# Performance work log

Hardware: AMD Instinct MI355X
Metric: run time of the kernel (lower is better)

## Reference

```python
import jax, jax.numpy as jnp
import numpy as np

K = 7
PAD = K // 2
SIG_L = (4.0, 6.0, 8.0)
SIG_S = (1.0, 2.0, 3.0)
DORD = (0, 1, 2)
ANG = (1, 2, 3, 4)
N_INV, N_EQ, N_CP = 8, 16, 16
LN_EPS = 1e-5


def _polar_grid(k):
    c = jnp.arange(k, dtype=jnp.float32) - (k - 1) / 2.0
    gy, gx = jnp.meshgrid(c, c, indexing='ij')
    r = jnp.sqrt(gx * gx + gy * gy + 1e-8)
    th = jnp.arctan2(gy, gx)
    return r, th


def _gaussian_basis(r, sigmas, orders, n):
    # Gaussian-derivative radial basis (Eqs. 13-14): cycle over (order, sigma) combos.
    combos = [(s, d) for d in orders for s in sigmas]
    mats = []
    for i in range(n):
        s, d = combos[i % len(combos)]
        u = r / s
        g = jnp.exp(-0.5 * u * u)
        p = jnp.ones_like(u) if d == 0 else (u if d == 1 else u * u - 1.0)
        psi = p * g
        mats.append(psi / jnp.sqrt(jnp.sum(psi * psi) + 1e-8))
    return jnp.stack(mats)  # [n, K, K]


def _harmonic_basis(r, th, w1, b1, w2, b2, n):
    # Circular harmonics (Eqs. 15-16): learnable radial MLP x cos/sin(n*theta).
    kk = r.size
    rad = jnp.tanh(r.reshape(kk, 1) @ w1 + b1) @ w2 + b2  # [K*K, M]
    tf = th.reshape(kk)
    ang = jnp.stack([f(o * tf) for o in ANG for f in (jnp.cos, jnp.sin)])  # [2L, K*K]
    basis = (rad.T[:, None, :] * ang[None, :, :]).reshape(-1, K, K)  # [M*2L, K, K]
    return basis[:n]


def _coeff(z, w1, b1, w2, b2, n, cout):
    h = jax.nn.relu(z @ w1 + b1)
    return (h @ w2 + b2).reshape(z.shape[0], n, cout)  # [B, N, C_out]


def _pconv(feature, kernel):
    # Per-sample kernel shared across input channels: conv2d with weight
    # expand over C_in == conv of the channel-sum with the per-(b,o) kernel.
    B, Cin, H, W = feature.shape
    Cout = kernel.shape[1]
    fs = feature.sum(axis=1)[None]  # [1, B, H, W]
    rhs = kernel.reshape(B * Cout, 1, K, K)
    out = jax.lax.conv_general_dilated(fs, rhs, (1, 1), [(PAD, PAD), (PAD, PAD)], feature_group_count=B)
    return out.reshape(B, Cout, H, W)


def _ln_c(x, g, b):
    # LayerNorm over channel dim (permute(0,2,3,1) -> LN -> permute back)
    mu = jnp.mean(x, axis=1, keepdims=True)
    var = jnp.var(x, axis=1, keepdims=True)
    return (x - mu) * jax.lax.rsqrt(var + LN_EPS) * g[None, :, None, None] + b[None, :, None, None]


def setup_inputs() -> dict:
    key = jax.random.key(0)
    ks = jax.random.split(key, 16)
    B, C, H, W = 16, 256, 48, 48
    hid = 64
    d = {}
    d['feature'] = jax.random.normal(ks[0], (B, C, H, W), jnp.float32)
    for i, (name, n) in enumerate([('inv', N_INV), ('eq', N_EQ), ('cp', N_CP)]):
        d[f'cg_{name}_w1'] = jax.random.normal(ks[1 + 4 * i], (C, hid), jnp.float32) * 0.05
        d[f'cg_{name}_b1'] = jnp.zeros((hid,), jnp.float32)
        d[f'cg_{name}_w2'] = jax.random.normal(ks[2 + 4 * i], (hid, n * C), jnp.float32) * 0.05
        d[f'cg_{name}_b2'] = jnp.zeros((n * C,), jnp.float32)
    d['rad_w1'] = jax.random.normal(ks[13], (1, 32), jnp.float32)
    d['rad_b1'] = jnp.zeros((32,), jnp.float32)
    d['rad_w2'] = jax.random.normal(ks[14], (32, 2), jnp.float32) * 0.3
    d['rad_b2'] = jnp.zeros((2,), jnp.float32)
    for name in ('inv', 'eq', 'cp'):
        d[f'ln_{name}_g'] = jnp.ones((C,), jnp.float32)
        d[f'ln_{name}_b'] = jnp.zeros((C,), jnp.float32)
    return d


def reference(feature, cg_inv_w1, cg_inv_b1, cg_inv_w2, cg_inv_b2,
              cg_eq_w1, cg_eq_b1, cg_eq_w2, cg_eq_b2,
              cg_cp_w1, cg_cp_b1, cg_cp_w2, cg_cp_b2,
              rad_w1, rad_b1, rad_w2, rad_b2,
              ln_inv_g, ln_inv_b, ln_eq_g, ln_eq_b, ln_cp_g, ln_cp_b):
    C_out = ln_inv_g.shape[0]
    r, th = _polar_grid(K)
    b_inv = _gaussian_basis(r, SIG_L, DORD, N_INV)
    b_eq = _gaussian_basis(r, SIG_S, DORD, N_EQ)
    b_cp = _harmonic_basis(r, th, rad_w1, rad_b1, rad_w2, rad_b2, N_CP)
    z = feature.mean(axis=(2, 3))  # [B, C] global average pool
    # Eq. 12: kernel[b,c] = sum_n coeff[b,n,c] * basis[n]
    k_inv = jnp.einsum('bnc,nhw->bchw', _coeff(z, cg_inv_w1, cg_inv_b1, cg_inv_w2, cg_inv_b2, N_INV, C_out), b_inv)
    k_eq = jnp.einsum('bnc,nhw->bchw', _coeff(z, cg_eq_w1, cg_eq_b1, cg_eq_w2, cg_eq_b2, N_EQ, C_out), b_eq)
    k_cp = jnp.einsum('bnc,nhw->bchw', _coeff(z, cg_cp_w1, cg_cp_b1, cg_cp_w2, cg_cp_b2, N_CP, C_out), b_cp)
    f_inv = _ln_c(_pconv(feature, k_inv), ln_inv_g, ln_inv_b)
    f_eq = _ln_c(_pconv(feature, k_eq), ln_eq_g, ln_eq_b)
    f_cp = _ln_c(_pconv(feature, k_cp), ln_cp_g, ln_cp_b)
    return (f_inv, f_eq, f_cp)
```

## Files before the change

### kernel.cpp

```cpp
#include <hip/hip_runtime.h>

#define B_ 16
#define C_ 256
#define H_ 48
#define W_ 48
#define HW_ 2304

typedef float f4 __attribute__((ext_vector_type(4)));

#define WS_ZPART 0
#define WS_FSPART 36864
#define WS_COEFFT 184320
#define WS_MQ 380928
#define WS_CMEAN 393216
#define WS_G 393984

__device__ __forceinline__ float wave_sum(float v) {
#pragma unroll
  for (int off = 32; off; off >>= 1) v += __shfl_xor(v, off, 64);
  return v;
}

__global__ __launch_bounds__(256) void zfs1_kernel(const float* __restrict__ feat,
                                                   float* __restrict__ zpart,
                                                   float* __restrict__ fspart) {
  int b = blockIdx.x, cc = blockIdx.y, pc = blockIdx.z;
  int tid = threadIdx.x;
  int p = pc * 256 + tid;
  const float* f = feat + ((size_t)b * C_ + cc * 64) * HW_ + p;
  __shared__ float zsum[256];
  int w = tid >> 6, lane = tid & 63;
  float facc = 0.f;
#pragma unroll 8
  for (int j = 0; j < 64; ++j) {
    float v = f[(size_t)j * HW_];
    facc += v;
    float s = wave_sum(v);
    if (lane == 0) zsum[w * 64 + j] = s;
  }
  fspart[cc * (B_ * HW_) + b * HW_ + p] = facc;
  __syncthreads();
  if (tid < 64) {
    float zv = zsum[tid] + zsum[64 + tid] + zsum[128 + tid] + zsum[192 + tid];
    zpart[((size_t)b * 256 + cc * 64 + tid) * 9 + pc] = zv;
  }
}

__global__ __launch_bounds__(256) void mid_kernel(
    const float* __restrict__ zpart, const float* __restrict__ fspart,
    const float* __restrict__ rw1, const float* __restrict__ rb1,
    const float* __restrict__ rw2, const float* __restrict__ rb2,
    const float* __restrict__ w1i, const float* __restrict__ b1i,
    const float* __restrict__ w2i, const float* __restrict__ b2i,
    const float* __restrict__ w1e, const float* __restrict__ b1e,
    const float* __restrict__ w2e, const float* __restrict__ b2e,
    const float* __restrict__ w1c, const float* __restrict__ b1c,
    const float* __restrict__ w2c, const float* __restrict__ b2c,
    float* __restrict__ G, float* __restrict__ coeffT,
    float* __restrict__ Mq, float* __restrict__ cmean) {
  __shared__ __align__(16) float smem[4672];
  int b = blockIdx.x, n = blockIdx.y, tid = threadIdx.x;
  if (n < 40) {
    float* fsp = smem;
    float* bas = smem + 3024;
    for (int i = tid; i < 3024; i += 256) {
      int y = i / 56 - 3;
      int x = i - (y + 3) * 56 - 3;
      float v = 0.f;
      if (y >= 0 && y < H_ && x >= 0 && x < W_) {
        int idx = b * HW_ + y * W_ + x;
        v = fspart[idx] + fspart[B_ * HW_ + idx] + fspart[2 * B_ * HW_ + idx] +
            fspart[3 * B_ * HW_ + idx];
      }
      fsp[i] = v;
    }
    if (tid < 64) {
      int t = tid;
      float r = 0.f, th = 0.f;
      if (t < 49) {
        int iy = t / 7, ix = t - iy * 7;
        float gy = (float)iy - 3.f, gx = (float)ix - 3.f;
        r = sqrtf(gx * gx + gy * gy + 1e-8f);
        th = atan2f(gy, gx);
      }
      if (n < 24) {
        const float SIGL[3] = {4.f, 6.f, 8.f};
        const float SIGS[3] = {1.f, 2.f, 3.f};
        int i = (n < 8) ? n : n - 8;
        int c = i % 9, d = c / 3;
        float s = (n < 8) ? SIGL[c % 3] : SIGS[c % 3];
        float p = 0.f;
        if (t < 49) {
          float u = r / s;
          float g = expf(-0.5f * u * u);
          p = ((d == 0) ? 1.f : ((d == 1) ? u : (u * u - 1.f))) * g;
        }
        float ss = wave_sum(p * p);
        if (t < 49) bas[t] = p / sqrtf(ss + 1e-8f);
      } else if (t < 49) {
        float r0 = rb2[0], r1 = rb2[1];
        for (int j = 0; j < 32; ++j) {
          float h = tanhf(r * rw1[j] + rb1[j]);
          r0 = fmaf(h, rw2[2 * j], r0);
          r1 = fmaf(h, rw2[2 * j + 1], r1);
        }
        int i = n - 24, m = i >> 3, a = i & 7, o = (a >> 1) + 1;
        float ang = (a & 1) ? sinf((float)o * th) : cosf((float)o * th);
        bas[t] = (m ? r1 : r0) * ang;
      }
    }
    __syncthreads();
    float kb[49];
#pragma unroll
    for (int i = 0; i < 49; ++i) kb[i] = bas[i];
    float* go = G + ((size_t)b * 40 + n) * HW_;
#pragma unroll
    for (int k = 0; k < 9; ++k) {
      int p = tid + k * 256;
      int y = p / 48, x = p - y * 48;
      float acc = 0.f;
#pragma unroll
      for (int dy = 0; dy < 7; ++dy)
#pragma unroll
        for (int dx = 0; dx < 7; ++dx)
          acc = fmaf(kb[dy * 7 + dx], fsp[(y + dy) * 56 + x + dx], acc);
      go[p] = acc;
    }
  } else {
    int branch = n - 40;
    int N = branch ? 16 : 8;
    const float* w1 = branch == 0 ? w1i : (branch == 1 ? w1e : w1c);
    const float* b1 = branch == 0 ? b1i : (branch == 1 ? b1e : b1c);
    const float* w2 = branch == 0 ? w2i : (branch == 1 ? w2e : w2c);
    const float* b2 = branch == 0 ? b2i : (branch == 1 ? b2e : b2c);
    float* zs = smem;
    float* hp = smem + 256;
    float* hs = smem + 512;
    float* Ls = smem + 576;
    {
      const float* zp = zpart + ((size_t)b * 256 + tid) * 9;
      float za = 0.f;
#pragma unroll
      for (int i = 0; i < 9; ++i) za += zp[i];
      zs[tid] = za * (1.f / (float)HW_);
    }
    __syncthreads();
    int j = tid & 63, part = tid >> 6;
    float acc = 0.f;
    const float* wp = w1 + part * 64 * 64 + j;
#pragma unroll 8
    for (int q = 0; q < 64; ++q) acc = fmaf(zs[part * 64 + q], wp[q * 64], acc);
    hp[tid] = acc;
    __syncthreads();
    if (tid < 64)
      hs[tid] = fmaxf(
          b1[tid] + hp[tid] + hp[64 + tid] + hp[128 + tid] + hp[192 + tid],
          0.f);
    __syncthreads();
    int c = tid;
    float cf[16];
    size_t stride = (size_t)N * 256;
#pragma unroll
    for (int nl = 0; nl < 16; ++nl) {
      float a = 0.f;
      if (nl < N) {
        a = b2[nl * 256 + c];
        const float* w2p = w2 + nl * 256 + c;
#pragma unroll 8
        for (int jj = 0; jj < 64; ++jj) a = fmaf(hs[jj], w2p[jj * stride], a);
      }
      cf[nl] = a;
      Ls[c * 16 + nl] = a;
    }
    float* ctp = coeffT + ((size_t)(b * 3 + branch) * 256 + c) * 16;
#pragma unroll
    for (int i = 0; i < 4; ++i)
      reinterpret_cast<f4*>(ctp)[i] = reinterpret_cast<const f4*>(cf)[i];
    __syncthreads();
    int nn = tid >> 4, mm = tid & 15;
    float dot = 0.f;
#pragma unroll 8
    for (int cc = 0; cc < 256; ++cc)
      dot = fmaf(Ls[cc * 16 + nn], Ls[cc * 16 + mm], dot);
    Mq[(b * 3 + branch) * 256 + tid] = dot * (1.f / 256.f);
    if (tid < 16) {
      float s = 0.f;
      for (int cc = 0; cc < 256; ++cc) s += Ls[cc * 16 + tid];
      cmean[(b * 3 + branch) * 16 + tid] = s * (1.f / 256.f);
    }
  }
}

__global__ __launch_bounds__(256) void pout_kernel(
    const float* __restrict__ G, const float* __restrict__ coeffT,
    const float* __restrict__ Mq, const float* __restrict__ cmean,
    const float* __restrict__ g0, const float* __restrict__ be0,
    const float* __restrict__ g1, const float* __restrict__ be1,
    const float* __restrict__ g2, const float* __restrict__ be2,
    float* __restrict__ out) {
  int branch = blockIdx.y;
  int bx = blockIdx.x;
  int b = bx / 72, pc = bx - b * 72;
  int p0 = pc * 32;
  int tid = threadIdx.x;
  int n0 = (branch == 0) ? 0 : ((branch == 1) ? 8 : 24);
  __shared__ __align__(16) float Ms[256];
  __shared__ float cms[16];
  __shared__ __align__(16) float smu[32];
  __shared__ __align__(16) float srs[32];
  Ms[tid] = Mq[(b * 3 + branch) * 256 + tid];
  if (tid < 16) cms[tid] = cmean[(b * 3 + branch) * 16 + tid];
  __syncthreads();
  if (tid < 32) {
    int p = p0 + tid;
    float gr[16];
#pragma unroll
    for (int n = 0; n < 16; ++n)
      gr[n] = G[((size_t)b * 40 + n0 + n) * HW_ + p];
    float mu = 0.f, q = 0.f;
#pragma unroll
    for (int n = 0; n < 16; ++n) {
      mu = fmaf(cms[n], gr[n], mu);
      float t = 0.f;
#pragma unroll
      for (int m = 0; m < 16; ++m) t = fmaf(Ms[n * 16 + m], gr[m], t);
      q = fmaf(gr[n], t, q);
    }
    smu[tid] = mu;
    srs[tid] = rsqrtf(q - mu * mu + 1e-5f);
  }
  __syncthreads();
  int pg = tid & 7, cg = tid >> 3;
  int p = p0 + pg * 4;
  f4 Gr[16];
#pragma unroll
  for (int n = 0; n < 16; ++n)
    Gr[n] = *reinterpret_cast<const f4*>(G + ((size_t)b * 40 + n0 + n) * HW_ + p);
  f4 mu4 = *reinterpret_cast<const f4*>(smu + pg * 4);
  f4 rs4 = *reinterpret_cast<const f4*>(srs + pg * 4);
  const float* gp = (branch == 0) ? g0 : ((branch == 1) ? g1 : g2);
  const float* bp = (branch == 0) ? be0 : ((branch == 1) ? be1 : be2);
  int c0 = cg * 8;
  float gch[8], bch[8];
#pragma unroll
  for (int i = 0; i < 8; ++i) {
    gch[i] = gp[c0 + i];
    bch[i] = bp[c0 + i];
  }
  const f4* ct4 =
      reinterpret_cast<const f4*>(coeffT + ((size_t)(b * 3 + branch) * 256 + c0) * 16);
  float* op = out + ((size_t)((branch * 16 + b) * 256 + c0)) * HW_ + p;
#pragma unroll
  for (int ci = 0; ci < 8; ++ci) {
    f4 a = ct4[ci * 4 + 0], bb = ct4[ci * 4 + 1];
    f4 cc = ct4[ci * 4 + 2], dd = ct4[ci * 4 + 3];
    f4 v = a.x * Gr[0];
    v += a.y * Gr[1];
    v += a.z * Gr[2];
    v += a.w * Gr[3];
    v += bb.x * Gr[4];
    v += bb.y * Gr[5];
    v += bb.z * Gr[6];
    v += bb.w * Gr[7];
    v += cc.x * Gr[8];
    v += cc.y * Gr[9];
    v += cc.z * Gr[10];
    v += cc.w * Gr[11];
    v += dd.x * Gr[12];
    v += dd.y * Gr[13];
    v += dd.z * Gr[14];
    v += dd.w * Gr[15];
    f4 o = (v - mu4) * rs4;
    o = o * gch[ci] + bch[ci];
    __builtin_nontemporal_store(o, reinterpret_cast<f4*>(op + (size_t)ci * HW_));
  }
}

extern "C" void kernel_launch(void* const* d_in, const int* in_sizes, int n_in,
                              void* d_out, int out_size, void* d_ws,
                              size_t ws_size, hipStream_t stream) {
  const float* feat = (const float*)d_in[0];
  float* ws = (float*)d_ws;
  float* zpart = ws + WS_ZPART;
  float* fspart = ws + WS_FSPART;
  float* coeffT = ws + WS_COEFFT;
  float* Mq = ws + WS_MQ;
  float* cmean = ws + WS_CMEAN;
  float* G = ws + WS_G;

  zfs1_kernel<<<dim3(16, 4, 9), 256, 0, stream>>>(feat, zpart, fspart);
  mid_kernel<<<dim3(16, 43), 256, 0, stream>>>(
      zpart, fspart, (const float*)d_in[13], (const float*)d_in[14],
      (const float*)d_in[15], (const float*)d_in[16], (const float*)d_in[1],
      (const float*)d_in[2], (const float*)d_in[3], (const float*)d_in[4],
      (const float*)d_in[5], (const float*)d_in[6], (const float*)d_in[7],
      (const float*)d_in[8], (const float*)d_in[9], (const float*)d_in[10],
      (const float*)d_in[11], (const float*)d_in[12], G, coeffT, Mq, cmean);
  pout_kernel<<<dim3(16 * 72, 3), 256, 0, stream>>>(
      G, coeffT, Mq, cmean, (const float*)d_in[17], (const float*)d_in[18],
      (const float*)d_in[19], (const float*)d_in[20], (const float*)d_in[21],
      (const float*)d_in[22], (float*)d_out);
}
```

Baseline: 309.0 us.

## Split basis/padded-sum prep into its own kernel and restructure basis convolution

Moves the padded channel-sum assembly and basis generation out of the per-(batch,basis) blocks into a separate small kernel that writes them once to workspace. The basis convolution now loads each pixel's 7x7 window into registers once and reuses it across 10 basis filters per block, instead of every block recomputing the padded map and basis. This removes 40x redundant fspart reads and basis math per batch, at the cost of an extra kernel launch and workspace round trip.

```diff
diff --git a/kernel.cpp b/kernel.cpp
--- a/kernel.cpp
+++ b/kernel.cpp
@@ -10,10 +10,12 @@
 
 #define WS_ZPART 0
 #define WS_FSPART 36864
-#define WS_COEFFT 184320
-#define WS_MQ 380928
-#define WS_CMEAN 393216
-#define WS_G 393984
+#define WS_FSPAD 184320
+#define WS_BASIS 232704
+#define WS_COEFFT 234784
+#define WS_MQ 431392
+#define WS_CMEAN 443680
+#define WS_G 444448
 
 __device__ __forceinline__ float wave_sum(float v) {
 #pragma unroll
@@ -46,10 +48,69 @@
   }
 }
 
-__global__ __launch_bounds__(256) void mid_kernel(
-    const float* __restrict__ zpart, const float* __restrict__ fspart,
-    const float* __restrict__ rw1, const float* __restrict__ rb1,
-    const float* __restrict__ rw2, const float* __restrict__ rb2,
+__global__ __launch_bounds__(256) void fsfin_kernel(
+    const float* __restrict__ fspart, const float* __restrict__ rw1,
+    const float* __restrict__ rb1, const float* __restrict__ rw2,
+    const float* __restrict__ rb2, float* __restrict__ fspad,
+    float* __restrict__ basis) {
+  int bx = blockIdx.x, tid = threadIdx.x;
+  if (bx < 16) {
+    int b = bx;
+    for (int i = tid; i < 54 * 56; i += 256) {
+      int yy = i / 56;
+      int xx = i - yy * 56;
+      int y = yy - 3, x = xx - 3;
+      float v = 0.f;
+      if (y >= 0 && y < H_ && x >= 0 && x < W_) {
+        int idx = b * HW_ + y * W_ + x;
+        v = fspart[idx] + fspart[B_ * HW_ + idx] + fspart[2 * B_ * HW_ + idx] +
+            fspart[3 * B_ * HW_ + idx];
+      }
+      fspad[b * 3024 + i] = v;
+    }
+    return;
+  }
+  if (tid >= 64) return;
+  int t = tid;
+  float r = 0.f, th = 0.f;
+  if (t < 49) {
+    int iy = t / 7, ix = t - iy * 7;
+    float gy = (float)iy - 3.f, gx = (float)ix - 3.f;
+    r = sqrtf(gx * gx + gy * gy + 1e-8f);
+    th = atan2f(gy, gx);
+  }
+  if (bx < 40) {
+    int f = bx - 16;
+    const float SIGL[3] = {4.f, 6.f, 8.f};
+    const float SIGS[3] = {1.f, 2.f, 3.f};
+    int i = (f < 8) ? f : f - 8;
+    int c = i % 9, d = c / 3;
+    float s = (f < 8) ? SIGL[c % 3] : SIGS[c % 3];
+    float p = 0.f;
+    if (t < 49) {
+      float u = r / s;
+      float g = expf(-0.5f * u * u);
+      p = ((d == 0) ? 1.f : ((d == 1) ? u : (u * u - 1.f))) * g;
+    }
+    float ss = wave_sum(p * p);
+    if (t < 49) basis[f * 52 + t] = p / sqrtf(ss + 1e-8f);
+  } else if (t < 49) {
+    int i = bx - 40;
+    float r0 = rb2[0], r1 = rb2[1];
+    for (int j = 0; j < 32; ++j) {
+      float h = tanhf(r * rw1[j] + rb1[j]);
+      r0 = fmaf(h, rw2[2 * j], r0);
+      r1 = fmaf(h, rw2[2 * j + 1], r1);
+    }
+    int m = i >> 3, a = i & 7, o = (a >> 1) + 1;
+    float ang = (a & 1) ? sinf((float)o * th) : cosf((float)o * th);
+    basis[(24 + i) * 52 + t] = (m ? r1 : r0) * ang;
+  }
+}
+
+__global__ __launch_bounds__(256) void gconv_kernel(
+    const float* __restrict__ fspad, const float* __restrict__ basis,
+    const float* __restrict__ zpart,
     const float* __restrict__ w1i, const float* __restrict__ b1i,
     const float* __restrict__ w2i, const float* __restrict__ b2i,
     const float* __restrict__ w1e, const float* __restrict__ b1e,
@@ -59,135 +120,89 @@
     float* __restrict__ G, float* __restrict__ coeffT,
     float* __restrict__ Mq, float* __restrict__ cmean) {
   __shared__ __align__(16) float smem[4672];
-  int b = blockIdx.x, n = blockIdx.y, tid = threadIdx.x;
-  if (n < 40) {
-    float* fsp = smem;
-    float* bas = smem + 3024;
-    for (int i = tid; i < 3024; i += 256) {
-      int y = i / 56 - 3;
-      int x = i - (y + 3) * 56 - 3;
-      float v = 0.f;
-      if (y >= 0 && y < H_ && x >= 0 && x < W_) {
-        int idx = b * HW_ + y * W_ + x;
-        v = fspart[idx] + fspart[B_ * HW_ + idx] + fspart[2 * B_ * HW_ + idx] +
-            fspart[3 * B_ * HW_ + idx];
-      }
-      fsp[i] = v;
-    }
-    if (tid < 64) {
-      int t = tid;
-      float r = 0.f, th = 0.f;
-      if (t < 49) {
-        int iy = t / 7, ix = t - iy * 7;
-        float gy = (float)iy - 3.f, gx = (float)ix - 3.f;
-        r = sqrtf(gx * gx + gy * gy + 1e-8f);
-        th = atan2f(gy, gx);
-      }
-      if (n < 24) {
-        const float SIGL[3] = {4.f, 6.f, 8.f};
-        const float SIGS[3] = {1.f, 2.f, 3.f};
-        int i = (n < 8) ? n : n - 8;
-        int c = i % 9, d = c / 3;
-        float s = (n < 8) ? SIGL[c % 3] : SIGS[c % 3];
-        float p = 0.f;
-        if (t < 49) {
-          float u = r / s;
-          float g = expf(-0.5f * u * u);
-          p = ((d == 0) ? 1.f : ((d == 1) ? u : (u * u - 1.f))) * g;
-        }
-        float ss = wave_sum(p * p);
-        if (t < 49) bas[t] = p / sqrtf(ss + 1e-8f);
-      } else if (t < 49) {
-        float r0 = rb2[0], r1 = rb2[1];
-        for (int j = 0; j < 32; ++j) {
-          float h = tanhf(r * rw1[j] + rb1[j]);
-          r0 = fmaf(h, rw2[2 * j], r0);
-          r1 = fmaf(h, rw2[2 * j + 1], r1);
-        }
-        int i = n - 24, m = i >> 3, a = i & 7, o = (a >> 1) + 1;
-        float ang = (a & 1) ? sinf((float)o * th) : cosf((float)o * th);
-        bas[t] = (m ? r1 : r0) * ang;
-      }
-    }
-    __syncthreads();
-    float kb[49];
-#pragma unroll
-    for (int i = 0; i < 49; ++i) kb[i] = bas[i];
-    float* go = G + ((size_t)b * 40 + n) * HW_;
-#pragma unroll
-    for (int k = 0; k < 9; ++k) {
-      int p = tid + k * 256;
-      int y = p / 48, x = p - y * 48;
+  int tid = threadIdx.x;
+  int ng = blockIdx.y;
+  if (ng < 4) {
+    int b = blockIdx.x / 9, pc = blockIdx.x - 9 * (blockIdx.x / 9);
+    int p = pc * 256 + tid;
+    int py = p / 48, px = p - py * 48;
+    const float* wb = fspad + b * 3024 + py * 56 + px;
+    float wreg[49];
+#pragma unroll
+    for (int dy = 0; dy < 7; ++dy)
+#pragma unroll
+      for (int dx = 0; dx < 7; ++dx) wreg[dy * 7 + dx] = wb[dy * 56 + dx];
+    float* go = G + ((size_t)b * 40 + ng * 10) * HW_ + p;
+#pragma unroll 2
+    for (int ni = 0; ni < 10; ++ni) {
+      const float* bs = basis + (ng * 10 + ni) * 52;
       float acc = 0.f;
 #pragma unroll
-      for (int dy = 0; dy < 7; ++dy)
-#pragma unroll
-        for (int dx = 0; dx < 7; ++dx)
-          acc = fmaf(kb[dy * 7 + dx], fsp[(y + dy) * 56 + x + dx], acc);
-      go[p] = acc;
-    }
-  } else {
-    int branch = n - 40;
-    int N = branch ? 16 : 8;
-    const float* w1 = branch == 0 ? w1i : (branch == 1 ? w1e : w1c);
-    const float* b1 = branch == 0 ? b1i : (branch == 1 ? b1e : b1c);
-    const float* w2 = branch == 0 ? w2i : (branch == 1 ? w2e : w2c);
-    const float* b2 = branch == 0 ? b2i : (branch == 1 ? b2e : b2c);
-    float* zs = smem;
-    float* hp = smem + 256;
-    float* hs = smem + 512;
-    float* Ls = smem + 576;
-    {
-      const float* zp = zpart + ((size_t)b * 256 + tid) * 9;
-      float za = 0.f;
-#pragma unroll
-      for (int i = 0; i < 9; ++i) za += zp[i];
-      zs[tid] = za * (1.f / (float)HW_);
-    }
-    __syncthreads();
-    int j = tid & 63, part = tid >> 6;
-    float acc = 0.f;
-    const float* wp = w1 + part * 64 * 64 + j;
+      for (int k = 0; k < 49; ++k) acc = fmaf(bs[k], wreg[k], acc);
+      go[(size_t)ni * HW_] = acc;
+    }
+    return;
+  }
+  if (blockIdx.x >= 48) return;
+  int b = blockIdx.x / 3, branch = blockIdx.x - 3 * b;
+  int N = branch ? 16 : 8;
+  const float* w1 = branch == 0 ? w1i : (branch == 1 ? w1e : w1c);
+  const float* b1 = branch == 0 ? b1i : (branch == 1 ? b1e : b1c);
+  const float* w2 = branch == 0 ? w2i : (branch == 1 ? w2e : w2c);
+  const float* b2 = branch == 0 ? b2i : (branch == 1 ? b2e : b2c);
+  float* zs = smem;
+  float* hp = smem + 256;
+  float* hs = smem + 512;
+  float* Ls = smem + 576;
+  {
+    const float* zp = zpart + ((size_t)b * 256 + tid) * 9;
+    float za = 0.f;
+#pragma unroll
+    for (int i = 0; i < 9; ++i) za += zp[i];
+    zs[tid] = za * (1.f / (float)HW_);
+  }
+  __syncthreads();
+  int j = tid & 63, part = tid >> 6;
+  float acc = 0.f;
+  const float* wp = w1 + part * 64 * 64 + j;
 #pragma unroll 8
-    for (int q = 0; q < 64; ++q) acc = fmaf(zs[part * 64 + q], wp[q * 64], acc);
-    hp[tid] = acc;
-    __syncthreads();
-    if (tid < 64)
-      hs[tid] = fmaxf(
-          b1[tid] + hp[tid] + hp[64 + tid] + hp[128 + tid] + hp[192 + tid],
-          0.f);
-    __syncthreads();
-    int c = tid;
-    float cf[16];
-    size_t stride = (size_t)N * 256;
-#pragma unroll
-    for (int nl = 0; nl < 16; ++nl) {
-      float a = 0.f;
-      if (nl < N) {
-        a = b2[nl * 256 + c];
-        const float* w2p = w2 + nl * 256 + c;
+  for (int q = 0; q < 64; ++q) acc = fmaf(zs[part * 64 + q], wp[q * 64], acc);
+  hp[tid] = acc;
+  __syncthreads();
+  if (tid < 64)
+    hs[tid] = fmaxf(
+        b1[tid] + hp[tid] + hp[64 + tid] + hp[128 + tid] + hp[192 + tid], 0.f);
+  __syncthreads();
+  int c = tid;
+  float cf[16];
+  size_t stride = (size_t)N * 256;
+#pragma unroll
+  for (int nl = 0; nl < 16; ++nl) {
+    float a = 0.f;
+    if (nl < N) {
+      a = b2[nl * 256 + c];
+      const float* w2p = w2 + nl * 256 + c;
 #pragma unroll 8
-        for (int jj = 0; jj < 64; ++jj) a = fmaf(hs[jj], w2p[jj * stride], a);
-      }
-      cf[nl] = a;
-      Ls[c * 16 + nl] = a;
-    }
-    float* ctp = coeffT + ((size_t)(b * 3 + branch) * 256 + c) * 16;
-#pragma unroll
-    for (int i = 0; i < 4; ++i)
-      reinterpret_cast<f4*>(ctp)[i] = reinterpret_cast<const f4*>(cf)[i];
-    __syncthreads();
-    int nn = tid >> 4, mm = tid & 15;
-    float dot = 0.f;
+      for (int jj = 0; jj < 64; ++jj) a = fmaf(hs[jj], w2p[jj * stride], a);
+    }
+    cf[nl] = a;
+    Ls[c * 16 + nl] = a;
+  }
+  float* ctp = coeffT + ((size_t)(b * 3 + branch) * 256 + c) * 16;
+#pragma unroll
+  for (int i = 0; i < 4; ++i)
+    reinterpret_cast<f4*>(ctp)[i] = reinterpret_cast<const f4*>(cf)[i];
+  __syncthreads();
+  int nn = tid >> 4, mm = tid & 15;
+  float dot = 0.f;
 #pragma unroll 8
-    for (int cc = 0; cc < 256; ++cc)
-      dot = fmaf(Ls[cc * 16 + nn], Ls[cc * 16 + mm], dot);
-    Mq[(b * 3 + branch) * 256 + tid] = dot * (1.f / 256.f);
-    if (tid < 16) {
-      float s = 0.f;
-      for (int cc = 0; cc < 256; ++cc) s += Ls[cc * 16 + tid];
-      cmean[(b * 3 + branch) * 16 + tid] = s * (1.f / 256.f);
-    }
+  for (int cc = 0; cc < 256; ++cc)
+    dot = fmaf(Ls[cc * 16 + nn], Ls[cc * 16 + mm], dot);
+  Mq[(b * 3 + branch) * 256 + tid] = dot * (1.f / 256.f);
+  if (tid < 16) {
+    float s = 0.f;
+    for (int cc = 0; cc < 256; ++cc) s += Ls[cc * 16 + tid];
+    cmean[(b * 3 + branch) * 16 + tid] = s * (1.f / 256.f);
   }
 }
 
@@ -283,19 +298,23 @@
   float* ws = (float*)d_ws;
   float* zpart = ws + WS_ZPART;
   float* fspart = ws + WS_FSPART;
+  float* fspad = ws + WS_FSPAD;
+  float* basis = ws + WS_BASIS;
   float* coeffT = ws + WS_COEFFT;
   float* Mq = ws + WS_MQ;
   float* cmean = ws + WS_CMEAN;
   float* G = ws + WS_G;
 
   zfs1_kernel<<<dim3(16, 4, 9), 256, 0, stream>>>(feat, zpart, fspart);
-  mid_kernel<<<dim3(16, 43), 256, 0, stream>>>(
-      zpart, fspart, (const float*)d_in[13], (const float*)d_in[14],
-      (const float*)d_in[15], (const float*)d_in[16], (const float*)d_in[1],
-      (const float*)d_in[2], (const float*)d_in[3], (const float*)d_in[4],
-      (const float*)d_in[5], (const float*)d_in[6], (const float*)d_in[7],
-      (const float*)d_in[8], (const float*)d_in[9], (const float*)d_in[10],
-      (const float*)d_in[11], (const float*)d_in[12], G, coeffT, Mq, cmean);
+  fsfin_kernel<<<56, 256, 0, stream>>>(
+      fspart, (const float*)d_in[13], (const float*)d_in[14],
+      (const float*)d_in[15], (const float*)d_in[16], fspad, basis);
+  gconv_kernel<<<dim3(144, 5), 256, 0, stream>>>(
+      fspad, basis, zpart, (const float*)d_in[1], (const float*)d_in[2],
+      (const float*)d_in[3], (const float*)d_in[4], (const float*)d_in[5],
+      (const float*)d_in[6], (const float*)d_in[7], (const float*)d_in[8],
+      (const float*)d_in[9], (const float*)d_in[10], (const float*)d_in[11],
+      (const float*)d_in[12], G, coeffT, Mq, cmean);
   pout_kernel<<<dim3(16 * 72, 3), 256, 0, stream>>>(
       G, coeffT, Mq, cmean, (const float*)d_in[17], (const float*)d_in[18],
       (const float*)d_in[19], (const float*)d_in[20], (const float*)d_in[21],
```

After: 319.1 us. 1.03x slower.
